# Performance work log

Measured on AMD Instinct MI355X. Metric: run time of the kernel, lower is better.

Reference implementation:

```python
import jax, jax.numpy as jnp
import numpy as np

DIM = 2048
N_HEADS = 16
Q_LORA = 1536
KV_LORA = 512
NOPE = 128
ROPE = 64
V_DIM = 128
QK_HEAD = NOPE + ROPE
SEQ = 4096
THETA = 10000.0
EPS = 1e-6
SCALE = QK_HEAD ** -0.5  # max_seq_len==4096 not >4096, so no mscale adjustment


def rms_norm(x, w):
    return x * jax.lax.rsqrt(jnp.mean(x * x, axis=-1, keepdims=True) + EPS) * w


def rope_cos_sin(seqlen):
    inv_freq = 1.0 / THETA ** (jnp.arange(0, ROPE, 2, dtype=jnp.float32) / ROPE)  # [ROPE/2]
    t = jnp.arange(seqlen, dtype=jnp.float32)
    freqs = jnp.outer(t, inv_freq)  # [S, ROPE/2]
    return jnp.cos(freqs), jnp.sin(freqs)


def apply_rope(x, cos, sin):
    # x: (b, s, h, ROPE); pairs (x0, x1) rotated as complex mult, interleaved layout
    b, s, h, d = x.shape
    xr = x.reshape(b, s, h, d // 2, 2)
    x0, x1 = xr[..., 0], xr[..., 1]
    c = cos[None, :, None, :]
    sn = sin[None, :, None, :]
    out = jnp.stack([x0 * c - x1 * sn, x0 * sn + x1 * c], axis=-1)
    return out.reshape(b, s, h, d)


def setup_inputs() -> dict:
    key = jax.random.key(0)
    ks = jax.random.split(key, 8)
    s = lambda fan_in: 1.0 / np.sqrt(fan_in)
    return {
        "x": jax.random.normal(ks[0], (1, SEQ, DIM), jnp.float32),
        "wq_a_w": jax.random.normal(ks[1], (Q_LORA, DIM), jnp.float32) * s(DIM),
        "q_norm_w": 1.0 + 0.02 * jax.random.normal(ks[2], (Q_LORA,), jnp.float32),
        "wq_b_w": jax.random.normal(ks[3], (N_HEADS * QK_HEAD, Q_LORA), jnp.float32) * s(Q_LORA),
        "wkv_a_w": jax.random.normal(ks[4], (KV_LORA + ROPE, DIM), jnp.float32) * s(DIM),
        "kv_norm_w": 1.0 + 0.02 * jax.random.normal(ks[5], (KV_LORA,), jnp.float32),
        "wkv_b_w": jax.random.normal(ks[6], (N_HEADS * (NOPE + V_DIM), KV_LORA), jnp.float32) * s(KV_LORA),
        "wo_w": jax.random.normal(ks[7], (DIM, DIM), jnp.float32) * s(DIM),
    }


def reference(x, wq_a_w, q_norm_w, wq_b_w, wkv_a_w, kv_norm_w, wkv_b_w, wo_w):
    b, seqlen, _ = x.shape
    cos, sin = rope_cos_sin(seqlen)

    # Q path: low-rank down-proj -> RMSNorm -> up-proj
    q = rms_norm(x @ wq_a_w.T, q_norm_w) @ wq_b_w.T
    q = q.reshape(b, seqlen, N_HEADS, QK_HEAD)
    q_nope, q_pe = q[..., :NOPE], q[..., NOPE:]
    q_pe = apply_rope(q_pe, cos, sin)

    # KV path: compressed latent + decoupled rope key
    kv_a = x @ wkv_a_w.T  # (b, s, KV_LORA + ROPE)
    kv_latent, k_pe_raw = kv_a[..., :KV_LORA], kv_a[..., KV_LORA:]
    kv = rms_norm(kv_latent, kv_norm_w)               # (b, t, c)
    k_pe = apply_rope(k_pe_raw[:, :, None, :], cos, sin)[:, :, 0, :]  # (b, t, r)

    # Absorption trick: fold wkv_b's K-part into q_nope, attend against latents
    wkv_b = wkv_b_w.reshape(N_HEADS, NOPE + V_DIM, KV_LORA)
    q_abs = jnp.einsum("bshd,hdc->bshc", q_nope, wkv_b[:, :NOPE])

    scores = (jnp.einsum("bshc,btc->bsht", q_abs, kv)
              + jnp.einsum("bshr,btr->bsht", q_pe, k_pe)) * SCALE

    # causal additive mask over (s_query, t_key)
    causal = jnp.tril(jnp.ones((seqlen, seqlen), dtype=bool))
    scores = jnp.where(causal[None, :, None, :], scores, jnp.float32(-1e30))
    attn = jax.nn.softmax(scores, axis=-1)

    # post-softmax: aggregate latents, then recover V via wkv_b's V-part
    ctx = jnp.einsum("bsht,btc->bshc", attn, kv)
    v = jnp.einsum("bshc,hdc->bshd", ctx, wkv_b[:, NOPE:])  # (b, s, h, V_DIM)
    out = v.reshape(b, seqlen, N_HEADS * V_DIM) @ wo_w.T
    return out
```

## Files before the change

kernel.cpp:

```cpp
#include <hip/hip_runtime.h>

typedef unsigned short u16;
typedef __attribute__((ext_vector_type(8))) short bf16x8;
typedef __attribute__((ext_vector_type(4))) float f32x4;
typedef __attribute__((ext_vector_type(4))) unsigned short u16x4;

#define MFMA16(a, b, c) __builtin_amdgcn_mfma_f32_16x16x32_bf16((a), (b), (c), 0, 0, 0)

#define SEQ 4096
#define SCALE 0.07216878364870323f
#define LOGTHETA 9.210340371976184f

__device__ __forceinline__ u16 f2bf(float f) {
  union { float f; unsigned u; } c; c.f = f;
  unsigned u = c.u;
  unsigned r = (u + 0x7fffu + ((u >> 16) & 1u)) >> 16;
  return (u16)r;
}
__device__ __forceinline__ float bf2f(u16 b) {
  union { unsigned u; float f; } c; c.u = ((unsigned)b) << 16;
  return c.f;
}

__global__ void cvt_all(const float* __restrict__ x, const float* __restrict__ wqa,
                        const float* __restrict__ wqb, const float* __restrict__ wkva,
                        const float* __restrict__ wkvb, const float* __restrict__ wo,
                        u16* __restrict__ xb, u16* __restrict__ wqab,
                        u16* __restrict__ wqbb, u16* __restrict__ wkvab,
                        u16* __restrict__ wkvbb, u16* __restrict__ wob) {
  const int e0 = 2097152;
  const int e1 = e0 + 786432;
  const int e2 = e1 + 1179648;
  const int e3 = e2 + 294912;
  const int e4 = e3 + 524288;
  const int e5 = e4 + 1048576;
  int stride = gridDim.x * blockDim.x;
  for (int i = blockIdx.x * blockDim.x + threadIdx.x; i < e5; i += stride) {
    const float* src; u16* dst; int j;
    if (i < e0)      { src = x;    dst = xb;    j = i; }
    else if (i < e1) { src = wqa;  dst = wqab;  j = i - e0; }
    else if (i < e2) { src = wqb;  dst = wqbb;  j = i - e1; }
    else if (i < e3) { src = wkva; dst = wkvab; j = i - e2; }
    else if (i < e4) { src = wkvb; dst = wkvbb; j = i - e3; }
    else             { src = wo;   dst = wob;   j = i - e4; }
    f32x4 v = ((const f32x4*)src)[j];
    u16x4 o;
    o[0] = f2bf(v[0]); o[1] = f2bf(v[1]); o[2] = f2bf(v[2]); o[3] = f2bf(v[3]);
    ((u16x4*)dst)[j] = o;
  }
}

__global__ void trans_wkvb(const float* __restrict__ w, u16* __restrict__ wt) {
  int stride = gridDim.x * blockDim.x;
  for (int i = blockIdx.x * blockDim.x + threadIdx.x; i < 16 * 512 * 128; i += stride) {
    int h = i >> 16;
    int r = i & 65535;
    int c = r >> 7, d = r & 127;
    wt[i] = f2bf(w[(h * 256 + d) * 512 + c]);
  }
}

__global__ void trans_vt(const u16* __restrict__ cc, u16* __restrict__ vt2) {
  __shared__ u16 tile[64][65];
  int c0 = blockIdx.x * 64;
  int t0 = blockIdx.y * 64;
  for (int k = 0; k < 16; k++) {
    int el = threadIdx.x + k * 256;
    int r = el >> 6, c = el & 63;
    tile[r][c] = cc[(t0 + r) * 2112 + 1536 + c0 + c];
  }
  __syncthreads();
  for (int k = 0; k < 16; k++) {
    int el = threadIdx.x + k * 256;
    int r = el >> 6, c = el & 63;
    int t = t0 + c;
    vt2[(t >> 5) * 16384 + (c0 + r) * 32 + (t & 31)] = tile[c][r];
  }
}

__global__ void rms_q_kernel(u16* __restrict__ cc, const float* __restrict__ w) {
  int row = blockIdx.x;
  u16* p = cc + (size_t)row * 2112;
  float vals[6];
  float ss = 0.f;
#pragma unroll
  for (int k = 0; k < 6; k++) {
    float v = bf2f(p[threadIdx.x + k * 256]);
    vals[k] = v;
    ss += v * v;
  }
  for (int m = 1; m < 64; m <<= 1) ss += __shfl_xor(ss, m);
  __shared__ float red[4];
  int wid = threadIdx.x >> 6;
  if ((threadIdx.x & 63) == 0) red[wid] = ss;
  __syncthreads();
  float tot = red[0] + red[1] + red[2] + red[3];
  float rr = rsqrtf(tot / 1536.f + 1e-6f);
#pragma unroll
  for (int k = 0; k < 6; k++) {
    int i = threadIdx.x + k * 256;
    p[i] = f2bf(vals[k] * rr * w[i]);
  }
}

__global__ void rms_kv_kernel(u16* __restrict__ cc, const float* __restrict__ w) {
  int t = blockIdx.x;
  u16* p = cc + (size_t)t * 2112 + 1536;
  float v0 = bf2f(p[threadIdx.x]);
  float v1 = bf2f(p[threadIdx.x + 256]);
  float ss = v0 * v0 + v1 * v1;
  for (int m = 1; m < 64; m <<= 1) ss += __shfl_xor(ss, m);
  __shared__ float red[4];
  int wid = threadIdx.x >> 6;
  if ((threadIdx.x & 63) == 0) red[wid] = ss;
  __syncthreads();
  float tot = red[0] + red[1] + red[2] + red[3];
  float rr = rsqrtf(tot / 512.f + 1e-6f);
  p[threadIdx.x] = f2bf(v0 * rr * w[threadIdx.x]);
  p[threadIdx.x + 256] = f2bf(v1 * rr * w[threadIdx.x + 256]);
  if (threadIdx.x < 32) {
    int i = threadIdx.x;
    float x0 = bf2f(p[512 + 2 * i]);
    float x1 = bf2f(p[512 + 2 * i + 1]);
    float invf = expf(-((float)(2 * i) / 64.f) * LOGTHETA);
    float ang = (float)t * invf;
    float cs = cosf(ang), sn = sinf(ang);
    p[512 + 2 * i] = f2bf(x0 * cs - x1 * sn);
    p[512 + 2 * i + 1] = f2bf(x0 * sn + x1 * cs);
  }
}

__global__ void rope_q_kernel(const u16* __restrict__ qb, u16* __restrict__ qcat) {
  int stride = gridDim.x * blockDim.x;
  for (int idx = blockIdx.x * blockDim.x + threadIdx.x; idx < 4096 * 512; idx += stride) {
    int s = idx >> 9;
    int r = idx & 511;
    int h = r >> 5, i = r & 31;
    float x0 = bf2f(qb[s * 3072 + h * 192 + 128 + 2 * i]);
    float x1 = bf2f(qb[s * 3072 + h * 192 + 128 + 2 * i + 1]);
    float invf = expf(-((float)(2 * i) / 64.f) * LOGTHETA);
    float ang = (float)s * invf;
    float cs = cosf(ang) * SCALE, sn = sinf(ang) * SCALE;
    qcat[s * 9216 + h * 576 + 512 + 2 * i] = f2bf(x0 * cs - x1 * sn);
    qcat[s * 9216 + h * 576 + 512 + 2 * i + 1] = f2bf(x0 * sn + x1 * cs);
  }
}

template <bool OUTF32>
__launch_bounds__(512, 2)
__global__ void gemm256(const u16* __restrict__ A, int lda,
                        const u16* __restrict__ W, int ldw,
                        void* __restrict__ Cp, int ldc, int K, float oscale,
                        int nvalid) {
  __shared__ __align__(16) u16 lds[2][32768];

  int wid = threadIdx.x >> 6, lane = threadIdx.x & 63;
  int quad = lane >> 4, l16 = lane & 15;
  int wr = wid >> 2, wc = wid & 3;
  int m0 = blockIdx.y * 256;
  int n0 = blockIdx.x * 256;

  f32x4 acc[8][4];
#pragma unroll
  for (int i = 0; i < 8; i++)
#pragma unroll
    for (int j = 0; j < 4; j++) acc[i][j] = {0.f, 0.f, 0.f, 0.f};

  const u16* sp[8];
  int soff[8];
#pragma unroll
  for (int jj = 0; jj < 8; jj++) {
    int c = jj * 8 + wid;
    soff[jj] = c * 512 + lane * 8;
    if (c < 32) {
      int rb = c >> 1, kh = c & 1;
      sp[jj] = A + (size_t)(m0 + rb * 16 + l16) * lda + kh * 32 + quad * 8;
    } else {
      int cb = c - 32, nb = cb >> 1, kh = cb & 1;
      int row = n0 + nb * 16 + l16;
      if (row >= nvalid) row = nvalid - 1;
      sp[jj] = W + (size_t)row * ldw + kh * 32 + quad * 8;
    }
  }

  int nkt = K >> 6;

#pragma unroll
  for (int jj = 0; jj < 8; jj++) {
    __builtin_amdgcn_global_load_lds(
        (const __attribute__((address_space(1))) unsigned int*)sp[jj],
        (__attribute__((address_space(3))) unsigned int*)&lds[0][soff[jj]], 16, 0, 0);
    sp[jj] += 64;
  }
  asm volatile("s_waitcnt vmcnt(0)" ::: "memory");
  __builtin_amdgcn_s_barrier();
  __builtin_amdgcn_sched_barrier(0);

  int buf = 0;
  for (int kt = 0; kt < nkt; kt++) {
    if (kt + 1 < nkt) {
#pragma unroll
      for (int jj = 0; jj < 8; jj++) {
        __builtin_amdgcn_global_load_lds(
            (const __attribute__((address_space(1))) unsigned int*)sp[jj],
            (__attribute__((address_space(3))) unsigned int*)&lds[buf ^ 1][soff[jj]], 16, 0, 0);
        sp[jj] += 64;
      }
    }
    const u16* base = &lds[buf][0];
#pragma unroll
    for (int kh = 0; kh < 2; kh++) {
      bf16x8 a[8], b[4];
#pragma unroll
      for (int i = 0; i < 8; i++)
        a[i] = *(const bf16x8*)(base + ((wr * 8 + i) * 2 + kh) * 512 + lane * 8);
#pragma unroll
      for (int j = 0; j < 4; j++)
        b[j] = *(const bf16x8*)(base + (32 + (wc * 4 + j) * 2 + kh) * 512 + lane * 8);
#pragma unroll
      for (int i = 0; i < 8; i++)
#pragma unroll
        for (int j = 0; j < 4; j++) acc[i][j] = MFMA16(a[i], b[j], acc[i][j]);
    }
    asm volatile("s_waitcnt vmcnt(0)" ::: "memory");
    __builtin_amdgcn_s_barrier();
    __builtin_amdgcn_sched_barrier(0);
    buf ^= 1;
  }

#pragma unroll
  for (int i = 0; i < 8; i++) {
    int row = m0 + wr * 128 + i * 16 + quad * 4;
#pragma unroll
    for (int j = 0; j < 4; j++) {
      int col = n0 + wc * 64 + j * 16 + l16;
      if (col < nvalid) {
#pragma unroll
        for (int r = 0; r < 4; r++) {
          size_t cbase = (size_t)(row + r) * ldc + col;
          if (OUTF32) ((float*)Cp)[cbase] = acc[i][j][r] * oscale;
          else        ((u16*)Cp)[cbase] = f2bf(acc[i][j][r] * oscale);
        }
      }
    }
  }
}

template <int BN, bool OUTF32>
__launch_bounds__(256)
__global__ void gemm_tiled(const u16* __restrict__ A, int lda, int az,
                           const u16* __restrict__ W, int ldw, int wz,
                           void* __restrict__ Cp, int ldc, int cz, int K, float oscale,
                           int nvalid) {
  constexpr int NCH = 8 + BN / 16;
  constexpr int NBF = BN / 32;
  __shared__ __align__(16) u16 lds[2][NCH * 512];

  int z = blockIdx.z;
  int wid = threadIdx.x >> 6, lane = threadIdx.x & 63;
  int quad = lane >> 4, l16 = lane & 15;
  int wr = wid >> 1, wc = wid & 1;
  int m0 = blockIdx.y * 128;
  int n0 = blockIdx.x * BN;

  const u16* Az = A + (size_t)z * az;
  const u16* Wz = W + (size_t)z * wz;

  f32x4 acc[4][NBF];
#pragma unroll
  for (int i = 0; i < 4; i++)
#pragma unroll
    for (int j = 0; j < NBF; j++) acc[i][j] = {0.f, 0.f, 0.f, 0.f};

#pragma unroll
  for (int jj = 0; jj < NCH / 4; jj++) {
    int c = jj * 4 + wid;
    const u16* src = (c < 8) ? (Az + (m0 + c * 16 + l16) * (size_t)lda + quad * 8)
                             : (Wz + (n0 + (c - 8) * 16 + l16) * (size_t)ldw + quad * 8);
    __builtin_amdgcn_global_load_lds(
        (const __attribute__((address_space(1))) unsigned int*)src,
        (__attribute__((address_space(3))) unsigned int*)&lds[0][c * 512], 16, 0, 0);
  }

  int buf = 0;
  for (int k0 = 0; k0 < K; k0 += 32) {
    __syncthreads();
    if (k0 + 32 < K) {
      int k1 = k0 + 32;
#pragma unroll
      for (int jj = 0; jj < NCH / 4; jj++) {
        int c = jj * 4 + wid;
        const u16* src = (c < 8) ? (Az + (m0 + c * 16 + l16) * (size_t)lda + k1 + quad * 8)
                                 : (Wz + (n0 + (c - 8) * 16 + l16) * (size_t)ldw + k1 + quad * 8);
        __builtin_amdgcn_global_load_lds(
            (const __attribute__((address_space(1))) unsigned int*)src,
            (__attribute__((address_space(3))) unsigned int*)&lds[buf ^ 1][c * 512], 16, 0, 0);
      }
    }
    const u16* base = &lds[buf][0];
    bf16x8 a[4], b[NBF];
#pragma unroll
    for (int i = 0; i < 4; i++)
      a[i] = *(const bf16x8*)(base + (wr * 4 + i) * 512 + lane * 8);
#pragma unroll
    for (int j = 0; j < NBF; j++)
      b[j] = *(const bf16x8*)(base + (8 + wc * NBF + j) * 512 + lane * 8);
#pragma unroll
    for (int i = 0; i < 4; i++)
#pragma unroll
      for (int j = 0; j < NBF; j++) acc[i][j] = MFMA16(a[i], b[j], acc[i][j]);
    buf ^= 1;
  }

#pragma unroll
  for (int i = 0; i < 4; i++) {
    int row = m0 + wr * 64 + i * 16 + quad * 4;
#pragma unroll
    for (int j = 0; j < NBF; j++) {
      int col = n0 + wc * (BN / 2) + j * 16 + l16;
      if (col < nvalid) {
#pragma unroll
        for (int r = 0; r < 4; r++) {
          size_t cbase = (size_t)z * cz + (size_t)(row + r) * ldc + col;
          if (OUTF32) ((float*)Cp)[cbase] = acc[i][j][r] * oscale;
          else        ((u16*)Cp)[cbase] = f2bf(acc[i][j][r] * oscale);
        }
      }
    }
  }
}

__launch_bounds__(512, 2)
__global__ void attn_kernel(const u16* __restrict__ qcat, const u16* __restrict__ kcat,
                            const u16* __restrict__ vt2, u16* __restrict__ ctx) {
  __shared__ __align__(16) u16 lds[2][34816];
  __shared__ __align__(16) u16 plds[8][16][40];

  int wid = threadIdx.x >> 6, lane = threadIdx.x & 63;
  int quad = lane >> 4, l16 = lane & 15;
  int bx = blockIdx.x;
  int h = bx & 15;
  int jb = 31 - (bx >> 4);
  int qb0 = jb << 7;
  int m0 = qb0 + wid * 16;

  bf16x8 q[18];
  {
    const u16* qb = qcat + (m0 + l16) * 9216 + h * 576 + quad * 8;
#pragma unroll
    for (int kk = 0; kk < 18; kk++) q[kk] = *(const bf16x8*)(qb + kk * 32);
  }

  f32x4 zero = {0.f, 0.f, 0.f, 0.f};
  f32x4 o[32];
#pragma unroll
  for (int ct = 0; ct < 32; ct++) o[ct] = zero;
  float li[4] = {0.f, 0.f, 0.f, 0.f};

  int nt = (qb0 >> 5) + 4;

  const u16* sp[9];
  int sstr[9], soff[9];
  bool sact[9];
#pragma unroll
  for (int jj = 0; jj < 9; jj++) {
    int c = jj * 8 + wid;
    sact[jj] = (c < 68);
    soff[jj] = c * 512;
    if (c < 36) {
      int kk = c >> 1, half = c & 1;
      sp[jj] = kcat + (half * 16 + l16) * 2112 + kk * 32 + quad * 8;
      sstr[jj] = 32 * 2112;
    } else {
      int ct = c - 36;
      sp[jj] = vt2 + (ct * 16 + l16) * 32 + quad * 8;
      sstr[jj] = 16384;
    }
  }

#pragma unroll
  for (int jj = 0; jj < 9; jj++) {
    if (sact[jj]) {
      __builtin_amdgcn_global_load_lds(
          (const __attribute__((address_space(1))) unsigned int*)sp[jj],
          (__attribute__((address_space(3))) unsigned int*)&lds[0][soff[jj]], 16, 0, 0);
      sp[jj] += sstr[jj];
    }
  }

  for (int ti = 0; ti < nt; ti++) {
    __syncthreads();
    int buf = ti & 1;
    if (ti + 1 < nt) {
      u16* dbase = &lds[buf ^ 1][0];
#pragma unroll
      for (int jj = 0; jj < 9; jj++) {
        if (sact[jj]) {
          __builtin_amdgcn_global_load_lds(
              (const __attribute__((address_space(1))) unsigned int*)sp[jj],
              (__attribute__((address_space(3))) unsigned int*)&dbase[soff[jj]], 16, 0, 0);
          sp[jj] += sstr[jj];
        }
      }
    }

    int t0 = ti << 5;
    if (t0 <= m0 + 15) {
      const u16* kb = &lds[buf][0];
      const u16* vb = &lds[buf][18432];
      f32x4 s0 = zero, s1 = zero;
#pragma unroll
      for (int kk = 0; kk < 18; kk++) {
        bf16x8 b0 = *(const bf16x8*)(&kb[(kk * 2 + 0) * 512 + lane * 8]);
        bf16x8 b1 = *(const bf16x8*)(&kb[(kk * 2 + 1) * 512 + lane * 8]);
        s0 = MFMA16(q[kk], b0, s0);
        s1 = MFMA16(q[kk], b1, s1);
      }
      int tc0 = t0 + l16, tc1 = t0 + 16 + l16;
#pragma unroll
      for (int r = 0; r < 4; r++) {
        int mrow = m0 + quad * 4 + r;
        float e0 = (tc0 <= mrow) ? __expf(s0[r]) : 0.f;
        float e1 = (tc1 <= mrow) ? __expf(s1[r]) : 0.f;
        li[r] += e0 + e1;
        plds[wid][quad * 4 + r][l16] = f2bf(e0);
        plds[wid][quad * 4 + r][16 + l16] = f2bf(e1);
      }
      __threadfence_block();
      bf16x8 ap = *(const bf16x8*)(&plds[wid][l16][quad * 8]);
#pragma unroll
      for (int ct = 0; ct < 32; ct++) {
        bf16x8 bv = *(const bf16x8*)(&vb[ct * 512 + lane * 8]);
        o[ct] = MFMA16(ap, bv, o[ct]);
      }
    }
  }

#pragma unroll
  for (int r = 0; r < 4; r++) {
    float s = li[r];
    s += __shfl_xor(s, 1);
    s += __shfl_xor(s, 2);
    s += __shfl_xor(s, 4);
    s += __shfl_xor(s, 8);
    li[r] = s;
  }
  f32x4 inv = {1.f / li[0], 1.f / li[1], 1.f / li[2], 1.f / li[3]};
#pragma unroll
  for (int ct = 0; ct < 32; ct++) {
    f32x4 val = o[ct] * inv;
    int base = (m0 + quad * 4) * 8192 + h * 512 + ct * 16 + l16;
    ctx[base] = f2bf(val[0]);
    ctx[base + 8192] = f2bf(val[1]);
    ctx[base + 2 * 8192] = f2bf(val[2]);
    ctx[base + 3 * 8192] = f2bf(val[3]);
  }
}

extern "C" void kernel_launch(void* const* d_in, const int* in_sizes, int n_in,
                              void* d_out, int out_size, void* d_ws, size_t ws_size,
                              hipStream_t stream) {
  const float* x = (const float*)d_in[0];
  const float* wqa = (const float*)d_in[1];
  const float* qnw = (const float*)d_in[2];
  const float* wqb = (const float*)d_in[3];
  const float* wkva = (const float*)d_in[4];
  const float* kvnw = (const float*)d_in[5];
  const float* wkvb = (const float*)d_in[6];
  const float* wo = (const float*)d_in[7];

  u16* ws = (u16*)d_ws;
  u16* XB = ws;
  u16* WQAB = ws + 8388608;
  u16* WKVAB = ws + 11534336;
  u16* WQBB = ws + 12713984;
  u16* WKVBB = ws + 17432576;
  u16* WKVBT = ws + 19529728;
  u16* WOB = ws + 20578304;
  u16* CC = ws + 24772608;
  u16* VT = ws + 33423360;
  u16* QCAT = ws + 35520512;
  u16* CTX = ws + 73269248;
  u16* QB = CTX;
  u16* VBUF = QCAT;

  dim3 blk(256);

  cvt_all<<<2048, blk, 0, stream>>>(x, wqa, wqb, wkva, wkvb, wo,
                                    XB, WQAB, WQBB, WKVAB, WKVBB, WOB);
  trans_wkvb<<<1024, blk, 0, stream>>>(wkvb, WKVBT);

  gemm256<false><<<dim3(9, 16), dim3(512), 0, stream>>>(
      XB, 2048, WQAB, 2048, CC, 2112, 2048, 1.f, 2112);

  rms_q_kernel<<<4096, blk, 0, stream>>>(CC, qnw);
  rms_kv_kernel<<<4096, blk, 0, stream>>>(CC, kvnw);
  trans_vt<<<dim3(8, 64), blk, 0, stream>>>(CC, VT);

  gemm256<false><<<dim3(12, 16), dim3(512), 0, stream>>>(
      CC, 2112, WQBB, 1536, QB, 3072, 1536, 1.f, 3072);

  gemm_tiled<128, false><<<dim3(4, 32, 16), blk, 0, stream>>>(
      QB, 3072, 192, WKVBT, 128, 65536, QCAT, 9216, 576, 128, SCALE, 1 << 30);
  rope_q_kernel<<<2048, blk, 0, stream>>>(QB, QCAT);

  attn_kernel<<<512, dim3(512), 0, stream>>>(QCAT, CC + 1536, VT, CTX);

  gemm_tiled<128, false><<<dim3(1, 32, 16), blk, 0, stream>>>(
      CTX, 8192, 512, WKVBB + 65536, 512, 131072, VBUF, 2048, 128, 512, 1.f, 1 << 30);

  gemm256<true><<<dim3(8, 16), dim3(512), 0, stream>>>(
      VBUF, 2048, WOB, 2048, d_out, 2048, 2048, 1.f, 2048);
}
```

Measured before the change: 909.2 us.

## Deepen gemm256 pipeline to 4-stage K=32 ring; tile-transpose wkv_b conversion

The 256x256 GEMM now loads K=32 slices into a four-buffer LDS ring, keeps three tiles in flight, and waits with partial vmcnt counts instead of draining every load each iteration. This is meant to hide global-load latency better than the old double buffer with K=64 steps. The trade-off is twice as many barriers per K, since there is one per 32-wide slice. Separately, the wkv_b transpose-and-convert kernel now goes through a shared-memory tile so both its reads and its writes are coalesced, replacing a strided gather.

```diff
diff --git a/kernel.cpp b/kernel.cpp
--- a/kernel.cpp
+++ b/kernel.cpp
@@ -51,12 +51,20 @@
 }
 
 __global__ void trans_wkvb(const float* __restrict__ w, u16* __restrict__ wt) {
-  int stride = gridDim.x * blockDim.x;
-  for (int i = blockIdx.x * blockDim.x + threadIdx.x; i < 16 * 512 * 128; i += stride) {
-    int h = i >> 16;
-    int r = i & 65535;
-    int c = r >> 7, d = r & 127;
-    wt[i] = f2bf(w[(h * 256 + d) * 512 + c]);
+  __shared__ float tile[64][65];
+  int c0 = blockIdx.x * 64;
+  int d0 = blockIdx.y * 64;
+  int h = blockIdx.z;
+  for (int k = 0; k < 16; k++) {
+    int el = threadIdx.x + k * 256;
+    int r = el >> 6, c = el & 63;
+    tile[r][c] = w[(h * 256 + d0 + r) * 512 + c0 + c];
+  }
+  __syncthreads();
+  for (int k = 0; k < 16; k++) {
+    int el = threadIdx.x + k * 256;
+    int r = el >> 6, c = el & 63;
+    wt[h * 65536 + (c0 + r) * 128 + d0 + c] = f2bf(tile[c][r]);
   }
 }
 
@@ -152,7 +160,7 @@
                         const u16* __restrict__ W, int ldw,
                         void* __restrict__ Cp, int ldc, int K, float oscale,
                         int nvalid) {
-  __shared__ __align__(16) u16 lds[2][32768];
+  __shared__ __align__(16) u16 lds[4][16384];
 
   int wid = threadIdx.x >> 6, lane = threadIdx.x & 63;
   int quad = lane >> 4, l16 = lane & 15;
@@ -166,66 +174,65 @@
 #pragma unroll
     for (int j = 0; j < 4; j++) acc[i][j] = {0.f, 0.f, 0.f, 0.f};
 
-  const u16* sp[8];
-  int soff[8];
-#pragma unroll
-  for (int jj = 0; jj < 8; jj++) {
+  const u16* sp[4];
+  int soff[4];
+#pragma unroll
+  for (int jj = 0; jj < 4; jj++) {
     int c = jj * 8 + wid;
     soff[jj] = c * 512 + lane * 8;
-    if (c < 32) {
-      int rb = c >> 1, kh = c & 1;
-      sp[jj] = A + (size_t)(m0 + rb * 16 + l16) * lda + kh * 32 + quad * 8;
+    if (c < 16) {
+      sp[jj] = A + (size_t)(m0 + c * 16 + l16) * lda + quad * 8;
     } else {
-      int cb = c - 32, nb = cb >> 1, kh = cb & 1;
-      int row = n0 + nb * 16 + l16;
+      int row = n0 + (c - 16) * 16 + l16;
       if (row >= nvalid) row = nvalid - 1;
-      sp[jj] = W + (size_t)row * ldw + kh * 32 + quad * 8;
-    }
-  }
-
-  int nkt = K >> 6;
-
-#pragma unroll
-  for (int jj = 0; jj < 8; jj++) {
-    __builtin_amdgcn_global_load_lds(
-        (const __attribute__((address_space(1))) unsigned int*)sp[jj],
-        (__attribute__((address_space(3))) unsigned int*)&lds[0][soff[jj]], 16, 0, 0);
-    sp[jj] += 64;
-  }
-  asm volatile("s_waitcnt vmcnt(0)" ::: "memory");
-  __builtin_amdgcn_s_barrier();
-  __builtin_amdgcn_sched_barrier(0);
-
-  int buf = 0;
+      sp[jj] = W + (size_t)row * ldw + quad * 8;
+    }
+  }
+
+  int nkt = K >> 5;
+
+#pragma unroll
+  for (int t = 0; t < 3; t++) {
+#pragma unroll
+    for (int jj = 0; jj < 4; jj++) {
+      __builtin_amdgcn_global_load_lds(
+          (const __attribute__((address_space(1))) unsigned int*)sp[jj],
+          (__attribute__((address_space(3))) unsigned int*)&lds[t][soff[jj]], 16, 0, 0);
+      sp[jj] += 32;
+    }
+  }
+
   for (int kt = 0; kt < nkt; kt++) {
-    if (kt + 1 < nkt) {
-#pragma unroll
-      for (int jj = 0; jj < 8; jj++) {
+    int rem = nkt - kt;
+    if (rem >= 3)      asm volatile("s_waitcnt vmcnt(8)" ::: "memory");
+    else if (rem == 2) asm volatile("s_waitcnt vmcnt(4)" ::: "memory");
+    else               asm volatile("s_waitcnt vmcnt(0)" ::: "memory");
+    __builtin_amdgcn_s_barrier();
+    __builtin_amdgcn_sched_barrier(0);
+
+    if (kt + 3 < nkt) {
+#pragma unroll
+      for (int jj = 0; jj < 4; jj++) {
         __builtin_amdgcn_global_load_lds(
             (const __attribute__((address_space(1))) unsigned int*)sp[jj],
-            (__attribute__((address_space(3))) unsigned int*)&lds[buf ^ 1][soff[jj]], 16, 0, 0);
-        sp[jj] += 64;
-      }
-    }
-    const u16* base = &lds[buf][0];
-#pragma unroll
-    for (int kh = 0; kh < 2; kh++) {
-      bf16x8 a[8], b[4];
-#pragma unroll
-      for (int i = 0; i < 8; i++)
-        a[i] = *(const bf16x8*)(base + ((wr * 8 + i) * 2 + kh) * 512 + lane * 8);
-#pragma unroll
-      for (int j = 0; j < 4; j++)
-        b[j] = *(const bf16x8*)(base + (32 + (wc * 4 + j) * 2 + kh) * 512 + lane * 8);
-#pragma unroll
-      for (int i = 0; i < 8; i++)
-#pragma unroll
-        for (int j = 0; j < 4; j++) acc[i][j] = MFMA16(a[i], b[j], acc[i][j]);
-    }
-    asm volatile("s_waitcnt vmcnt(0)" ::: "memory");
-    __builtin_amdgcn_s_barrier();
-    __builtin_amdgcn_sched_barrier(0);
-    buf ^= 1;
+            (__attribute__((address_space(3))) unsigned int*)&lds[(kt + 3) & 3][soff[jj]],
+            16, 0, 0);
+        sp[jj] += 32;
+      }
+    }
+
+    const u16* base = &lds[kt & 3][0];
+    bf16x8 a[8], b[4];
+#pragma unroll
+    for (int i = 0; i < 8; i++)
+      a[i] = *(const bf16x8*)(base + (wr * 8 + i) * 512 + lane * 8);
+#pragma unroll
+    for (int j = 0; j < 4; j++)
+      b[j] = *(const bf16x8*)(base + (16 + wc * 4 + j) * 512 + lane * 8);
+#pragma unroll
+    for (int i = 0; i < 8; i++)
+#pragma unroll
+      for (int j = 0; j < 4; j++) acc[i][j] = MFMA16(a[i], b[j], acc[i][j]);
   }
 
 #pragma unroll
@@ -488,7 +495,7 @@
 
   cvt_all<<<2048, blk, 0, stream>>>(x, wqa, wqb, wkva, wkvb, wo,
                                     XB, WQAB, WQBB, WKVAB, WKVBB, WOB);
-  trans_wkvb<<<1024, blk, 0, stream>>>(wkvb, WKVBT);
+  trans_wkvb<<<dim3(8, 2, 16), blk, 0, stream>>>(wkvb, WKVBT);
 
   gemm256<false><<<dim3(9, 16), dim3(512), 0, stream>>>(
       XB, 2048, WQAB, 2048, CC, 2112, 2048, 1.f, 2112);
```

Measured after the change: 858.7 us. 1.06x faster.
